# Kernel tuning notes

Hardware: AMD Instinct MI355X
Metric: run time of the kernel (lower is better)

The kernel has to match this reference:

```python
import jax, jax.numpy as jnp
import numpy as np

DROPOUT_P = 0.1  # original source passed p=1 (degenerate, zeros output); 0.1 used for a meaningful baseline


def setup_inputs() -> dict:
    key0 = jax.random.key(0)
    ks = jax.random.split(key0, 11)
    B, H, L, D, DQK, DV = 2, 8, 2048, 1024, 64, 64
    return {
        "query": jax.random.normal(ks[0], (B, H, L, D), jnp.float32),
        "key":   jax.random.normal(ks[1], (B, H, L, D), jnp.float32),
        "value": jax.random.normal(ks[2], (B, H, L, D), jnp.float32),
        "Wq": jax.random.normal(ks[3], (D, DQK), jnp.float32) * (D ** -0.5),
        "bq": jax.random.normal(ks[4], (DQK,), jnp.float32) * 0.02,
        "Wk": jax.random.normal(ks[5], (D, DQK), jnp.float32) * (D ** -0.5),
        "bk": jax.random.normal(ks[6], (DQK,), jnp.float32) * 0.02,
        "Wv": jax.random.normal(ks[7], (D, DV), jnp.float32) * (D ** -0.5),
        "bv": jax.random.normal(ks[8], (DV,), jnp.float32) * 0.02,
        "Wo": jax.random.normal(ks[9], (DV, D), jnp.float32) * (DV ** -0.5),
        "bo": jax.random.normal(ks[10], (D,), jnp.float32) * 0.02,
    }


def reference(query, key, value, Wq, bq, Wk, bk, Wv, bv, Wo, bo):
    # Per-head linear projections on 4D inputs (B,H,L,d_model)
    q = query @ Wq + bq            # (B,H,Lq,dqk)
    k = key @ Wk + bk              # (B,H,Lk,dqk)
    v = value @ Wv + bv            # (B,H,Lk,dv)
    # Quirky scale from source: q.size(2)*q.size(3)/key.size(2) * key.size(-1)**-0.5
    dk = (q.shape[2] * q.shape[3] / key.shape[2]) * (key.shape[-1] ** -0.5)
    scores = jnp.einsum('bhqd,bhkd->bhqk', q, k) * jnp.float32(dk)
    attn = jax.nn.softmax(scores, axis=-1)
    # Deterministic dropout with fixed key (inverted-scale, matching F.dropout)
    keep = jax.random.bernoulli(jax.random.key(42), 1.0 - DROPOUT_P, attn.shape)
    attn = jnp.where(keep, attn / (1.0 - DROPOUT_P), jnp.float32(0.0))
    out = jnp.einsum('bhqk,bhkd->bhqd', attn, v)  # (B,H,Lq,dv)
    return out @ Wo + bo                           # (B,H,Lq,d_model)
```

## Files before the change

kernel.cpp:

```cpp
#include <hip/hip_runtime.h>
#include <stdint.h>

typedef _Float16 f16;
typedef __attribute__((ext_vector_type(8))) _Float16 f16x8;
typedef __attribute__((ext_vector_type(4))) float f32x4;

__device__ __forceinline__ uint32_t rotl1(uint32_t x, uint32_t n){
  return __builtin_amdgcn_alignbit(x, x, 32u - n);
}
__device__ __forceinline__ uint32_t tf_bits(uint32_t i){
  const uint32_t ks1 = 42u, ks2 = 0x1BD11BDAu ^ 42u;
  uint32_t x0 = 0u, x1 = i + 42u;
#define R4(a,b,c,d) \
  x0 += x1; x1 = rotl1(x1,a); x1 ^= x0; \
  x0 += x1; x1 = rotl1(x1,b); x1 ^= x0; \
  x0 += x1; x1 = rotl1(x1,c); x1 ^= x0; \
  x0 += x1; x1 = rotl1(x1,d); x1 ^= x0;
  R4(13,15,26,6)  x0 += ks1; x1 += ks2 + 1u;
  R4(17,29,16,24) x0 += ks2; x1 += 2u;
  R4(13,15,26,6)               x1 += ks1 + 3u;
  R4(17,29,16,24) x0 += ks1; x1 += ks2 + 4u;
  R4(13,15,26,6)  x0 += ks2; x1 += 5u;
#undef R4
  return x0 ^ x1;
}

__global__ __launch_bounds__(256) void proj_kernel(
    const float* __restrict__ query, const float* __restrict__ keyp, const float* __restrict__ value,
    const float* __restrict__ Wq, const float* __restrict__ bq,
    const float* __restrict__ Wk, const float* __restrict__ bk,
    const float* __restrict__ Wv, const float* __restrict__ bv,
    const float* __restrict__ Wo,
    f16* __restrict__ qp, f16* __restrict__ kp, f16* __restrict__ vpT,
    f16* __restrict__ WoT)
{
  __shared__ __align__(16) f16 Alds[64][40];
  __shared__ __align__(16) f16 Wlds[64][40];
  const int bid = blockIdx.x;
  const int tid = threadIdx.x;
  const int lane = tid & 63, wave = tid >> 6;
  const int llo = lane & 15, lhi = lane >> 4;

  if (bid >= 1536){
    int t = (bid - 1536)*256 + tid;
    int n = t & 1023, k = t >> 10;
    WoT[(long)n*64 + k] = (f16)Wo[(long)k*1024 + n];
    return;
  }

  const int p = bid;
  const int which = p >> 9;
  const long m0 = (long)(p & 511) * 64;
  const float* A    = which==0 ? query : (which==1 ? keyp : value);
  const float* W    = which==0 ? Wq    : (which==1 ? Wk   : Wv);
  const float* bias = which==0 ? bq    : (which==1 ? bk   : bv);

  f32x4 acc[4];
  #pragma unroll
  for (int n=0;n<4;n++){
    float bb = bias[16*n + llo];
    acc[n][0]=bb; acc[n][1]=bb; acc[n][2]=bb; acc[n][3]=bb;
  }

  const int ar = tid >> 2;
  const int ac = (tid & 3) * 8;
  const int wcol = tid & 63;
  const int wk = (tid >> 6) * 8;

  for (int k0 = 0; k0 < 1024; k0 += 32){
    {
      const float* asrc = A + (m0 + ar)*1024 + k0 + ac;
      float4 v0 = *(const float4*)asrc;
      float4 v1 = *(const float4*)(asrc + 4);
      union { f16 h[8]; f16x8 v; } aw;
      aw.h[0]=(f16)v0.x; aw.h[1]=(f16)v0.y; aw.h[2]=(f16)v0.z; aw.h[3]=(f16)v0.w;
      aw.h[4]=(f16)v1.x; aw.h[5]=(f16)v1.y; aw.h[6]=(f16)v1.z; aw.h[7]=(f16)v1.w;
      *(f16x8*)&Alds[ar][ac] = aw.v;
      f16 wt[8];
      #pragma unroll
      for (int j=0;j<8;j++) wt[j] = (f16)W[(long)(k0+wk+j)*64 + wcol];
      *(f16x8*)&Wlds[wcol][wk] = *(f16x8*)wt;
    }
    __syncthreads();
    f16x8 af = *(const f16x8*)&Alds[wave*16 + llo][lhi*8];
    #pragma unroll
    for (int n=0;n<4;n++){
      f16x8 bf = *(const f16x8*)&Wlds[16*n + llo][lhi*8];
      acc[n] = __builtin_amdgcn_mfma_f32_16x16x32_f16(af, bf, acc[n], 0,0,0);
    }
    __syncthreads();
  }

  if (which < 2){
    const float scale = (which==0) ? 2.0f : 1.0f;
    f16* dst = (which==0) ? qp : kp;
    #pragma unroll
    for (int n=0;n<4;n++)
      #pragma unroll
      for (int j=0;j<4;j++){
        long row = m0 + wave*16 + lhi*4 + j;
        dst[row*64 + 16*n + llo] = (f16)(acc[n][j]*scale);
      }
  } else {
    long row0 = m0 + wave*16 + lhi*4;
    long bh = row0 >> 11;
    long lr = row0 & 2047;
    #pragma unroll
    for (int n=0;n<4;n++){
      union { f16 h[4]; ushort4 u; } pk;
      #pragma unroll
      for (int j=0;j<4;j++) pk.h[j] = (f16)acc[n][j];
      *(ushort4*)&vpT[(bh*64 + 16*n + llo)*2048 + lr] = pk.u;
    }
  }
}

__global__ __launch_bounds__(256) void flash_kernel(
    const f16* __restrict__ qp, const f16* __restrict__ kp, const f16* __restrict__ vpT,
    const f16* __restrict__ WoT, const float* __restrict__ bo, float* __restrict__ out)
{
  __shared__ __align__(16) f16 Klds[64][72];
  __shared__ __align__(16) f16 Vlds[64][72];
  __shared__ __align__(16) f16 Plds[4][16][72];
  __shared__ unsigned short Idl[4][1024];
  const int tid = threadIdx.x;
  const int lane = tid & 63, wave = tid >> 6;
  const int llo = lane & 15, lhi = lane >> 4;
  const int bh = blockIdx.y;
  const int q0 = blockIdx.x * 64;

  const f16* qbase = qp + ((long)bh*2048 + q0 + wave*16 + llo)*64 + lhi*8;
  f16x8 qf0 = *(const f16x8*)qbase;
  f16x8 qf1 = *(const f16x8*)(qbase + 32);

  f32x4 O[4];
  float mrun[4], lrun[4];
  #pragma unroll
  for (int n=0;n<4;n++){ O[n][0]=0.f;O[n][1]=0.f;O[n][2]=0.f;O[n][3]=0.f; }
  #pragma unroll
  for (int j=0;j<4;j++){ mrun[j] = -__builtin_inff(); lrun[j]=0.f; }

  const int sr = tid >> 2;
  const int sc = (tid & 3) * 16;
  const f16* kbh = kp + (long)bh*2048*64;
  const f16* vbh = vpT + (long)bh*64*2048;
  uint32_t base_w = (uint32_t)((bh*2048 + q0 + wave*16)*2048);

  for (int kv0 = 0; kv0 < 2048; kv0 += 64, base_w += 64u){
    {
      const f16* src = kbh + (long)(kv0 + sr)*64 + sc;
      f16x8 t0 = *(const f16x8*)src;
      f16x8 t1 = *(const f16x8*)(src+8);
      *(f16x8*)&Klds[sr][sc]   = t0;
      *(f16x8*)&Klds[sr][sc+8] = t1;
      const f16* vsrc = vbh + (long)sr*2048 + kv0 + sc;
      f16x8 u0 = *(const f16x8*)vsrc;
      f16x8 u1 = *(const f16x8*)(vsrc+8);
      *(f16x8*)&Vlds[sr][sc]   = u0;
      *(f16x8*)&Vlds[sr][sc+8] = u1;
    }
    __syncthreads();

    f32x4 s[4];
    #pragma unroll
    for (int n=0;n<4;n++){ s[n][0]=0.f;s[n][1]=0.f;s[n][2]=0.f;s[n][3]=0.f; }
    #pragma unroll
    for (int n=0;n<4;n++){
      f16x8 kf0 = *(const f16x8*)&Klds[16*n+llo][lhi*8];
      s[n] = __builtin_amdgcn_mfma_f32_16x16x32_f16(qf0, kf0, s[n], 0,0,0);
      f16x8 kf1 = *(const f16x8*)&Klds[16*n+llo][32+lhi*8];
      s[n] = __builtin_amdgcn_mfma_f32_16x16x32_f16(qf1, kf1, s[n], 0,0,0);
    }
    float pmax[4];
    #pragma unroll
    for (int j=0;j<4;j++)
      pmax[j] = fmaxf(fmaxf(s[0][j],s[1][j]), fmaxf(s[2][j],s[3][j]));
    #pragma unroll
    for (int off=1; off<16; off<<=1){
      #pragma unroll
      for (int j=0;j<4;j++) pmax[j] = fmaxf(pmax[j], __shfl_xor(pmax[j], off));
    }
    float esc[4];
    #pragma unroll
    for (int j=0;j<4;j++){
      float mnew = fmaxf(mrun[j], pmax[j]);
      esc[j] = __expf(mrun[j] - mnew);
      mrun[j] = mnew;
    }
    float p[4][4]; float lsum[4] = {0.f,0.f,0.f,0.f};
    #pragma unroll
    for (int n=0;n<4;n++)
      #pragma unroll
      for (int j=0;j<4;j++){
        p[n][j] = __expf(s[n][j] - mrun[j]);
        lsum[j] += p[n][j];
      }
    #pragma unroll
    for (int off=1; off<16; off<<=1){
      #pragma unroll
      for (int j=0;j<4;j++) lsum[j] += __shfl_xor(lsum[j], off);
    }
    #pragma unroll
    for (int j=0;j<4;j++) lrun[j] = lrun[j]*esc[j] + lsum[j];
    #pragma unroll
    for (int n=0;n<4;n++)
      #pragma unroll
      for (int j=0;j<4;j++) O[n][j] *= esc[j];

    uint32_t cnt = 0;
    #pragma unroll
    for (int j=0;j<4;j++){
      #pragma unroll
      for (int n=0;n<4;n++){
        float pm = p[n][j]*(1.0f/0.9f);
        bool surv = pm > 0x1.0p-25f;
        Plds[wave][lhi*4+j][16*n+llo] = (f16)pm;
        unsigned long long mk = __ballot(surv);
        if (mk){
          uint32_t pre = __builtin_amdgcn_mbcnt_hi((uint32_t)(mk>>32),
                         __builtin_amdgcn_mbcnt_lo((uint32_t)mk, 0u));
          if (surv)
            Idl[wave][cnt + pre] = (unsigned short)((j<<8)|(n<<6)|lane);
          cnt += (uint32_t)__builtin_popcountll(mk);
        }
      }
    }
    for (uint32_t pb = 0; pb < cnt; pb += 64){
      uint32_t idx = pb + (uint32_t)lane;
      if (idx < cnt){
        uint32_t id = (uint32_t)Idl[wave][idx];
        uint32_t jj = (id>>8)&3u, nn = (id>>6)&3u, ln = id & 63u;
        uint32_t i = base_w + (ln>>4)*8192u + jj*2048u + nn*16u + (ln&15u);
        uint32_t bits = tf_bits(i);
        if (bits >= 0xE6666600u)
          Plds[wave][(ln>>4)*4+jj][16*nn+(ln&15u)] = (f16)0;
      }
    }

    f16x8 pa0 = *(const f16x8*)&Plds[wave][llo][lhi*8];
    f16x8 pa1 = *(const f16x8*)&Plds[wave][llo][32+lhi*8];
    #pragma unroll
    for (int n=0;n<4;n++){
      f16x8 vf0 = *(const f16x8*)&Vlds[16*n+llo][lhi*8];
      O[n] = __builtin_amdgcn_mfma_f32_16x16x32_f16(pa0, vf0, O[n], 0,0,0);
      f16x8 vf1 = *(const f16x8*)&Vlds[16*n+llo][32+lhi*8];
      O[n] = __builtin_amdgcn_mfma_f32_16x16x32_f16(pa1, vf1, O[n], 0,0,0);
    }
    __syncthreads();
  }

  float rl[4];
  #pragma unroll
  for (int j=0;j<4;j++) rl[j] = 1.0f / lrun[j];
  #pragma unroll
  for (int n=0;n<4;n++)
    #pragma unroll
    for (int j=0;j<4;j++)
      Klds[wave*16 + lhi*4 + j][16*n + llo] = (f16)(O[n][j]*rl[j]);
  __syncthreads();

  f16x8 af0 = *(const f16x8*)&Klds[wave*16 + llo][lhi*8];
  f16x8 af1 = *(const f16x8*)&Klds[wave*16 + llo][32 + lhi*8];
  const long robase = (long)bh*2048 + q0 + wave*16 + lhi*4;
  for (int n0 = 0; n0 < 1024; n0 += 16){
    f16x8 b0 = *(const f16x8*)&WoT[(long)(n0+llo)*64 + lhi*8];
    f16x8 b1 = *(const f16x8*)&WoT[(long)(n0+llo)*64 + 32 + lhi*8];
    float bb = bo[n0+llo];
    f32x4 c; c[0]=bb; c[1]=bb; c[2]=bb; c[3]=bb;
    c = __builtin_amdgcn_mfma_f32_16x16x32_f16(af0, b0, c, 0,0,0);
    c = __builtin_amdgcn_mfma_f32_16x16x32_f16(af1, b1, c, 0,0,0);
    #pragma unroll
    for (int j=0;j<4;j++)
      out[(robase + j)*1024 + n0 + llo] = c[j];
  }
}

extern "C" void kernel_launch(void* const* d_in, const int* in_sizes, int n_in,
                              void* d_out, int out_size, void* d_ws, size_t ws_size,
                              hipStream_t stream){
  const float* query = (const float*)d_in[0];
  const float* key   = (const float*)d_in[1];
  const float* value = (const float*)d_in[2];
  const float* Wq = (const float*)d_in[3];
  const float* bq = (const float*)d_in[4];
  const float* Wk = (const float*)d_in[5];
  const float* bk = (const float*)d_in[6];
  const float* Wv = (const float*)d_in[7];
  const float* bv = (const float*)d_in[8];
  const float* Wo = (const float*)d_in[9];
  const float* bo = (const float*)d_in[10];
  float* out = (float*)d_out;

  char* ws = (char*)d_ws;
  f16* qp   = (f16*)(ws);
  f16* kp   = (f16*)(ws + ((size_t)4<<20));
  f16* vpT  = (f16*)(ws + ((size_t)8<<20));
  f16* WoT  = (f16*)(ws + ((size_t)20<<20));

  proj_kernel<<<dim3(1792), dim3(256), 0, stream>>>(
      query,key,value,Wq,bq,Wk,bk,Wv,bv,Wo,qp,kp,vpT,WoT);
  flash_kernel<<<dim3(32,16), dim3(256), 0, stream>>>(qp,kp,vpT,WoT,bo,out);
}
```

Measured before the change: 254.8 us.

## Pre-transpose weights to fp16 and stream projection operands directly into registers

Adds a small kernel that converts and transposes Wq/Wk/Wv/Wo to fp16 once per call. The projection kernel then drops its LDS staging and barriers, loading A rows and transposed weight fragments straight from global memory into MFMA registers with double-buffered prefetch across k-steps. This targets the strided scalar weight loads, per-tile fp16 conversion and barrier stalls in the memory-bound projection. The cost is an extra kernel launch and weight fragments read redundantly from L2 by every block.

```diff
diff --git a/kernel.cpp b/kernel.cpp
--- a/kernel.cpp
+++ b/kernel.cpp
@@ -25,36 +25,68 @@
   return x0 ^ x1;
 }
 
+__global__ __launch_bounds__(256) void wt_kernel(
+    const float* __restrict__ Wq, const float* __restrict__ Wk,
+    const float* __restrict__ Wv, const float* __restrict__ Wo,
+    f16* __restrict__ WqT, f16* __restrict__ WkT,
+    f16* __restrict__ WvT, f16* __restrict__ WoT)
+{
+  __shared__ __align__(16) f16 Tl[64][72];
+  const int b = blockIdx.x, tid = threadIdx.x;
+  const int which = b >> 4, t = b & 15;
+  const float* src = which==0?Wq:(which==1?Wk:(which==2?Wv:Wo));
+  const int rr = tid >> 2, cb = (tid & 3) * 16;
+  if (which < 3){
+    const float* s = src + (long)(t*64 + rr)*64 + cb;
+    #pragma unroll
+    for (int j=0;j<16;j++) Tl[cb+j][rr] = (f16)s[j];
+  } else {
+    const float* s = src + (long)rr*1024 + t*64 + cb;
+    #pragma unroll
+    for (int j=0;j<16;j++) Tl[cb+j][rr] = (f16)s[j];
+  }
+  __syncthreads();
+  f16* dst = which==0?WqT:(which==1?WkT:(which==2?WvT:WoT));
+  const int c = tid >> 2, kb = (tid & 3) * 16;
+  if (which < 3){
+    *(f16x8*)&dst[(long)c*1024 + t*64 + kb]     = *(const f16x8*)&Tl[c][kb];
+    *(f16x8*)&dst[(long)c*1024 + t*64 + kb + 8] = *(const f16x8*)&Tl[c][kb+8];
+  } else {
+    *(f16x8*)&dst[(long)(t*64 + c)*64 + kb]     = *(const f16x8*)&Tl[c][kb];
+    *(f16x8*)&dst[(long)(t*64 + c)*64 + kb + 8] = *(const f16x8*)&Tl[c][kb+8];
+  }
+}
+
+__device__ __forceinline__ void proj_step(const float4* ab, const f16x8* wb, f32x4* acc){
+  union { f16 h[8]; f16x8 v; } u0, u1;
+  u0.h[0]=(f16)ab[0].x; u0.h[1]=(f16)ab[0].y; u0.h[2]=(f16)ab[0].z; u0.h[3]=(f16)ab[0].w;
+  u0.h[4]=(f16)ab[1].x; u0.h[5]=(f16)ab[1].y; u0.h[6]=(f16)ab[1].z; u0.h[7]=(f16)ab[1].w;
+  u1.h[0]=(f16)ab[2].x; u1.h[1]=(f16)ab[2].y; u1.h[2]=(f16)ab[2].z; u1.h[3]=(f16)ab[2].w;
+  u1.h[4]=(f16)ab[3].x; u1.h[5]=(f16)ab[3].y; u1.h[6]=(f16)ab[3].z; u1.h[7]=(f16)ab[3].w;
+  #pragma unroll
+  for (int n=0;n<4;n++){
+    acc[n] = __builtin_amdgcn_mfma_f32_16x16x32_f16(u0.v, wb[n*2],   acc[n], 0,0,0);
+    acc[n] = __builtin_amdgcn_mfma_f32_16x16x32_f16(u1.v, wb[n*2+1], acc[n], 0,0,0);
+  }
+}
+
 __global__ __launch_bounds__(256) void proj_kernel(
     const float* __restrict__ query, const float* __restrict__ keyp, const float* __restrict__ value,
-    const float* __restrict__ Wq, const float* __restrict__ bq,
-    const float* __restrict__ Wk, const float* __restrict__ bk,
-    const float* __restrict__ Wv, const float* __restrict__ bv,
-    const float* __restrict__ Wo,
-    f16* __restrict__ qp, f16* __restrict__ kp, f16* __restrict__ vpT,
-    f16* __restrict__ WoT)
+    const f16* __restrict__ WqT, const f16* __restrict__ WkT, const f16* __restrict__ WvT,
+    const float* __restrict__ bq, const float* __restrict__ bk, const float* __restrict__ bv,
+    f16* __restrict__ qp, f16* __restrict__ kp, f16* __restrict__ vpT)
 {
-  __shared__ __align__(16) f16 Alds[64][40];
-  __shared__ __align__(16) f16 Wlds[64][40];
   const int bid = blockIdx.x;
+  const int which = bid >> 9;
+  const long m0 = (long)(bid & 511) * 64;
+  const float* A    = which==0 ? query : (which==1 ? keyp : value);
+  const f16*   WT   = which==0 ? WqT   : (which==1 ? WkT  : WvT);
+  const float* bias = which==0 ? bq    : (which==1 ? bk   : bv);
+
   const int tid = threadIdx.x;
   const int lane = tid & 63, wave = tid >> 6;
   const int llo = lane & 15, lhi = lane >> 4;
 
-  if (bid >= 1536){
-    int t = (bid - 1536)*256 + tid;
-    int n = t & 1023, k = t >> 10;
-    WoT[(long)n*64 + k] = (f16)Wo[(long)k*1024 + n];
-    return;
-  }
-
-  const int p = bid;
-  const int which = p >> 9;
-  const long m0 = (long)(p & 511) * 64;
-  const float* A    = which==0 ? query : (which==1 ? keyp : value);
-  const float* W    = which==0 ? Wq    : (which==1 ? Wk   : Wv);
-  const float* bias = which==0 ? bq    : (which==1 ? bk   : bv);
-
   f32x4 acc[4];
   #pragma unroll
   for (int n=0;n<4;n++){
@@ -62,34 +94,31 @@
     acc[n][0]=bb; acc[n][1]=bb; acc[n][2]=bb; acc[n][3]=bb;
   }
 
-  const int ar = tid >> 2;
-  const int ac = (tid & 3) * 8;
-  const int wcol = tid & 63;
-  const int wk = (tid >> 6) * 8;
-
-  for (int k0 = 0; k0 < 1024; k0 += 32){
-    {
-      const float* asrc = A + (m0 + ar)*1024 + k0 + ac;
-      float4 v0 = *(const float4*)asrc;
-      float4 v1 = *(const float4*)(asrc + 4);
-      union { f16 h[8]; f16x8 v; } aw;
-      aw.h[0]=(f16)v0.x; aw.h[1]=(f16)v0.y; aw.h[2]=(f16)v0.z; aw.h[3]=(f16)v0.w;
-      aw.h[4]=(f16)v1.x; aw.h[5]=(f16)v1.y; aw.h[6]=(f16)v1.z; aw.h[7]=(f16)v1.w;
-      *(f16x8*)&Alds[ar][ac] = aw.v;
-      f16 wt[8];
-      #pragma unroll
-      for (int j=0;j<8;j++) wt[j] = (f16)W[(long)(k0+wk+j)*64 + wcol];
-      *(f16x8*)&Wlds[wcol][wk] = *(f16x8*)wt;
-    }
-    __syncthreads();
-    f16x8 af = *(const f16x8*)&Alds[wave*16 + llo][lhi*8];
-    #pragma unroll
-    for (int n=0;n<4;n++){
-      f16x8 bf = *(const f16x8*)&Wlds[16*n + llo][lhi*8];
-      acc[n] = __builtin_amdgcn_mfma_f32_16x16x32_f16(af, bf, acc[n], 0,0,0);
-    }
-    __syncthreads();
-  }
+  const float* arow = A + (m0 + wave*16 + llo)*1024 + lhi*8;
+  const f16*   wrow = WT + (long)llo*1024 + lhi*8;
+
+#define LOADA(k0, d) { \
+    d[0] = *(const float4*)(arow + (k0)); \
+    d[1] = *(const float4*)(arow + (k0) + 4); \
+    d[2] = *(const float4*)(arow + (k0) + 32); \
+    d[3] = *(const float4*)(arow + (k0) + 36); }
+#define LOADW(k0, d) { \
+    _Pragma("unroll") \
+    for (int n=0;n<4;n++){ \
+      d[n*2]   = *(const f16x8*)(wrow + n*16384 + (k0)); \
+      d[n*2+1] = *(const f16x8*)(wrow + n*16384 + (k0) + 32); } }
+
+  float4 a0[4], a1[4]; f16x8 w0[8], w1[8];
+  LOADA(0, a0) LOADW(0, w0)
+  #pragma unroll 1
+  for (int it = 0; it < 16; it += 2){
+    LOADA((it+1)*64, a1) LOADW((it+1)*64, w1)
+    proj_step(a0, w0, acc);
+    if (it + 2 < 16){ LOADA((it+2)*64, a0) LOADW((it+2)*64, w0) }
+    proj_step(a1, w1, acc);
+  }
+#undef LOADA
+#undef LOADW
 
   if (which < 2){
     const float scale = (which==0) ? 2.0f : 1.0f;
@@ -296,8 +325,12 @@
   f16* kp   = (f16*)(ws + ((size_t)4<<20));
   f16* vpT  = (f16*)(ws + ((size_t)8<<20));
   f16* WoT  = (f16*)(ws + ((size_t)20<<20));
-
-  proj_kernel<<<dim3(1792), dim3(256), 0, stream>>>(
-      query,key,value,Wq,bq,Wk,bk,Wv,bv,Wo,qp,kp,vpT,WoT);
+  f16* WqT  = (f16*)(ws + ((size_t)21<<20));
+  f16* WkT  = (f16*)(ws + ((size_t)21<<20) + (256<<10));
+  f16* WvT  = (f16*)(ws + ((size_t)21<<20) + (512<<10));
+
+  wt_kernel<<<dim3(64), dim3(256), 0, stream>>>(Wq,Wk,Wv,Wo,WqT,WkT,WvT,WoT);
+  proj_kernel<<<dim3(1536), dim3(256), 0, stream>>>(
+      query,key,value,WqT,WkT,WvT,bq,bk,bv,qp,kp,vpT);
   flash_kernel<<<dim3(32,16), dim3(256), 0, stream>>>(qp,kp,vpT,WoT,bo,out);
 }
```

Result: slower. 285.2 us (+12.0%).
